# Performance work log

Measured on AMD Instinct MI355X. Metric: run time of the kernel, lower is better.

Reference implementation:

```python
import jax, jax.numpy as jnp
import numpy as np

HIDDEN = 4096
N_HEADS = 32
N_KV_HEADS = 8
HEAD_DIM = HIDDEN // N_HEADS          # 128
GROUP = N_HEADS // N_KV_HEADS         # 4 q-heads per kv-head
Q_SIZE = N_HEADS * HEAD_DIM           # 4096
KV_SIZE = N_KV_HEADS * HEAD_DIM       # 1024
T = 2048


def setup_inputs() -> dict:
    key = jax.random.key(0)
    k1, k2, k3 = jax.random.split(key, 3)
    positions = jnp.arange(T, dtype=jnp.int64) if jax.config.jax_enable_x64 else jnp.arange(T, dtype=jnp.int32)
    hidden_states = jax.random.normal(k1, (T, HIDDEN), dtype=jnp.float32)
    # torch.nn.Linear weights: out = x @ W.T
    w_qkv = jax.random.normal(k2, (Q_SIZE + 2 * KV_SIZE, HIDDEN), dtype=jnp.float32) * 0.02
    w_o = jax.random.normal(k3, (HIDDEN, HIDDEN), dtype=jnp.float32) * 0.02
    return {"positions": positions, "hidden_states": hidden_states, "w_qkv": w_qkv, "w_o": w_o}


def reference(positions, hidden_states, w_qkv, w_o):
    del positions  # rotary is a no-op in the fake module
    t = hidden_states.shape[0]
    scaling = HEAD_DIM ** -0.5

    qkv = hidden_states @ w_qkv.T                              # [T, q+2kv]
    q, k, v = jnp.split(qkv, [Q_SIZE, Q_SIZE + KV_SIZE], axis=-1)
    # GQA mapping: q-head h uses kv-head h // GROUP (contiguous groups)
    q = q.reshape(t, N_KV_HEADS, GROUP, HEAD_DIM)              # [T, Hkv, G, d]
    k = k.reshape(t, N_KV_HEADS, HEAD_DIM)                     # [T, Hkv, d]
    v = v.reshape(t, N_KV_HEADS, HEAD_DIM)

    # Cache starts empty -> token i attends to keys 0..i (causal prefill)
    logits = jnp.einsum('tkgd,skd->kgts', q, k) * scaling      # [Hkv, G, T, T]
    causal = jnp.tril(jnp.ones((t, t), dtype=bool))            # s <= t
    logits = jnp.where(causal, logits, jnp.finfo(logits.dtype).min)
    weights = jax.nn.softmax(logits, axis=-1)
    ctx = jnp.einsum('kgts,skd->tkgd', weights, v)             # [T, Hkv, G, d]
    ctx = ctx.reshape(t, HIDDEN)
    return ctx @ w_o.T
```

## Files before the change

kernel.cpp:

```cpp
#include <hip/hip_runtime.h>

typedef unsigned short u16;
typedef __bf16 bf16x8 __attribute__((ext_vector_type(8)));
typedef float f32x4 __attribute__((ext_vector_type(4)));

__device__ __forceinline__ u16 f2bf(float f) {
  union { float f; unsigned u; } v; v.f = f;
  unsigned r = v.u + 0x7FFFu + ((v.u >> 16) & 1u);
  return (u16)(r >> 16);
}

__device__ __forceinline__ u16 bfc(float f) {
  __bf16 h = (__bf16)f;
  return *(u16*)&h;
}

__device__ __forceinline__ void gload16(const void* g, void* l) {
  __builtin_amdgcn_global_load_lds(
      (const __attribute__((address_space(1))) unsigned int*)g,
      (__attribute__((address_space(3))) unsigned int*)l, 16, 0, 0);
}

__global__ __launch_bounds__(256) void cvt_bf16(const float* __restrict__ in,
                                                u16* __restrict__ out, long n) {
  long i = ((long)blockIdx.x * 256 + threadIdx.x) * 8;
  const long stride = (long)gridDim.x * 2048;
  for (; i < n; i += stride) {
    float4 a = *(const float4*)(in + i);
    float4 b = *(const float4*)(in + i + 4);
    uint4 o;
    o.x = (unsigned)f2bf(a.x) | ((unsigned)f2bf(a.y) << 16);
    o.y = (unsigned)f2bf(a.z) | ((unsigned)f2bf(a.w) << 16);
    o.z = (unsigned)f2bf(b.x) | ((unsigned)f2bf(b.y) << 16);
    o.w = (unsigned)f2bf(b.z) | ((unsigned)f2bf(b.w) << 16);
    *(uint4*)(out + i) = o;
  }
}

__global__ __launch_bounds__(256) void pack_b(const float* __restrict__ w,
                                              u16* __restrict__ out, int kb32) {
  const int tid = threadIdx.x;
  const int unit = blockIdx.x * 4 + (tid >> 6);
  const int ln = tid & 63, lr = ln & 15, lg = ln >> 4;
  const int n16 = unit / kb32, k32 = unit % kb32;
  const float* src = w + (size_t)(n16 * 16 + lr) * (kb32 * 32) + k32 * 32 + lg * 8;
  float4 a = *(const float4*)src;
  float4 b = *(const float4*)(src + 4);
  uint4 o;
  o.x = (unsigned)f2bf(a.x) | ((unsigned)f2bf(a.y) << 16);
  o.y = (unsigned)f2bf(a.z) | ((unsigned)f2bf(a.w) << 16);
  o.z = (unsigned)f2bf(b.x) | ((unsigned)f2bf(b.y) << 16);
  o.w = (unsigned)f2bf(b.z) | ((unsigned)f2bf(b.w) << 16);
  *(uint4*)(out + (size_t)unit * 512 + ln * 8) = o;
}

template <int BN, typename OUT>
__global__ __launch_bounds__(256) void gemmV(const u16* __restrict__ A,
                                             const u16* __restrict__ Bp,
                                             OUT* __restrict__ C,
                                             int M, int N, int K) {
  constexpr int BM = 128;
  constexpr int MREP = 4;
  constexpr int NREP = BN / 32;
  constexpr int AI = 4;
  __shared__ __align__(16) u16 sA[2][BM * 64];

  const int tid = threadIdx.x;
  const int w = tid >> 6, ln = tid & 63;
  const int lr = ln & 15, lg = ln >> 4;
  const int wr = w >> 1, wc = w & 1;

  const int bid = (int)blockIdx.x;
  const int bm = (bid & 15) * BM;
  const int bn = (bid >> 4) * BN;

  const int srow = tid >> 3;
  const int scol = (((tid & 7) * 16) ^ ((srow & 7) << 4)) >> 1;
  const u16* pA = A + (size_t)(bm + srow) * K + scol;

  const int mask = (lr & 7) << 4;
  const int pAr = (wr * 64 + lr) * 128;
  const int kb32 = K >> 5;
  const u16* pB = Bp + ((size_t)((bn >> 4) + wc * NREP)) * kb32 * 512 + ln * 8;

  f32x4 acc[MREP][NREP] = {};
  const int nk = K >> 6;

  auto stageA = [&](int buf, int t) {
    const int k0 = t << 6;
#pragma unroll
    for (int i = 0; i < AI; ++i)
      gload16(pA + (size_t)i * 32 * K + k0, (char*)sA[buf] + i * 4096 + tid * 16);
  };
  auto loadB = [&](bf16x8 (&br)[NREP][2], int t) {
#pragma unroll
    for (int nf = 0; nf < NREP; ++nf)
#pragma unroll
      for (int s = 0; s < 2; ++s)
        br[nf][s] = *(const bf16x8*)(pB + ((size_t)nf * kb32 + 2 * t + s) * 512);
  };

  bf16x8 b[NREP][2];
  stageA(0, 0);
  loadB(b, 0);

#pragma unroll 1
  for (int t = 0; t < nk; ++t) {
    const int buf = t & 1;
    const char* lA = (const char*)sA[buf];
    const bool more = (t + 1 < nk);

    asm volatile("s_waitcnt vmcnt(0)" ::: "memory");
    __builtin_amdgcn_sched_barrier(0);
    __builtin_amdgcn_s_barrier();
    __builtin_amdgcn_sched_barrier(0);
    if (more) stageA(buf ^ 1, t + 1);

    bf16x8 af[MREP][2];
#pragma unroll
    for (int m = 0; m < MREP; ++m)
      af[m][0] = *(const bf16x8*)(lA + pAr + m * 2048 + ((lg * 16) ^ mask));
#pragma unroll
    for (int m = 0; m < MREP; ++m)
      af[m][1] = *(const bf16x8*)(lA + pAr + m * 2048 + ((lg * 16 + 64) ^ mask));

    asm volatile("s_waitcnt lgkmcnt(%0)" :: "n"(MREP) : "memory");
    __builtin_amdgcn_sched_barrier(0);
    __builtin_amdgcn_s_setprio(1);
#pragma unroll
    for (int m = 0; m < MREP; ++m)
#pragma unroll
      for (int nf = 0; nf < NREP; ++nf)
        acc[m][nf] = __builtin_amdgcn_mfma_f32_16x16x32_bf16(
            af[m][0], b[nf][0], acc[m][nf], 0, 0, 0);
    __builtin_amdgcn_s_setprio(0);
    asm volatile("s_waitcnt lgkmcnt(0)" ::: "memory");
    __builtin_amdgcn_sched_barrier(0);
    __builtin_amdgcn_s_setprio(1);
#pragma unroll
    for (int m = 0; m < MREP; ++m)
#pragma unroll
      for (int nf = 0; nf < NREP; ++nf)
        acc[m][nf] = __builtin_amdgcn_mfma_f32_16x16x32_bf16(
            af[m][1], b[nf][1], acc[m][nf], 0, 0, 0);
    __builtin_amdgcn_s_setprio(0);

    if (more) loadB(b, t + 1);
  }

#pragma unroll
  for (int m = 0; m < MREP; ++m)
#pragma unroll
    for (int nf = 0; nf < NREP; ++nf)
#pragma unroll
      for (int r = 0; r < 4; ++r) {
        const int row = bm + wr * 64 + m * 16 + lg * 4 + r;
        const int col = bn + wc * (BN / 2) + nf * 16 + lr;
        const float v = acc[m][nf][r];
        if constexpr (sizeof(OUT) == 2)
          C[(size_t)row * N + col] = (OUT)bfc(v);
        else
          C[(size_t)row * N + col] = v;
      }
}

__global__ __launch_bounds__(256) void vtrans(const u16* __restrict__ qkv,
                                              u16* __restrict__ vT) {
  __shared__ u16 tile[128][65];
  const int hk = blockIdx.y;
  const int tb = blockIdx.x * 64;
  const int tid = threadIdx.x;
#pragma unroll
  for (int p = 0; p < 4; ++p) {
    const int tr = p * 16 + (tid >> 4);
    const int d0 = (tid & 15) * 8;
    const uint4 x = *(const uint4*)(qkv + (size_t)(tb + tr) * 6144 + 5120 + hk * 128 + d0);
    const u16* xv = (const u16*)&x;
#pragma unroll
    for (int j = 0; j < 8; ++j) tile[d0 + j][tr] = xv[j];
  }
  __syncthreads();
#pragma unroll
  for (int p = 0; p < 4; ++p) {
    const int d = p * 32 + (tid >> 3);
    const int t0 = (tid & 7) * 8;
    u16 v[8];
#pragma unroll
    for (int j = 0; j < 8; ++j) v[j] = tile[d][t0 + j];
    uint4 o;
    unsigned* ov = (unsigned*)&o;
#pragma unroll
    for (int j = 0; j < 4; ++j)
      ov[j] = (unsigned)v[2 * j] | ((unsigned)v[2 * j + 1] << 16);
    *(uint4*)(vT + (size_t)hk * 128 * 2048 + (size_t)d * 2048 + tb + t0) = o;
  }
}

__global__ __launch_bounds__(256) void attn(const u16* __restrict__ qkv,
                                            const u16* __restrict__ vT,
                                            u16* __restrict__ ctx) {
  __shared__ __align__(16) u16 sK[2][64 * 128];
  __shared__ __align__(16) u16 sV[2][128 * 64];
  __shared__ __align__(16) u16 sP[4 * 16 * 64];
  const int tid = threadIdx.x, w = tid >> 6, ln = tid & 63;
  const int lr = ln & 15, lg = ln >> 4;
  const int h = blockIdx.y, hk = h >> 2;
  const int pi = blockIdx.x;

  const float Cs = 0.12751737f;
  char* const pw = (char*)sP + w * 2048;

  auto stage = [&](int buf, int kt) {
    const int kvbase = kt * 64;
#pragma unroll
    for (int i = 0; i < 4; ++i) {
      const int off = i * 4096 + tid * 16;
      {
        const int row = off >> 8, cbp = off & 255;
        const int cb = cbp ^ ((row & 7) << 4);
        gload16(qkv + (size_t)(kvbase + row) * 6144 + 4096 + hk * 128 + (cb >> 1),
                (char*)sK + buf * 16384 + off);
      }
      {
        const int row = off >> 7, cbp = off & 127;
        const int cb = cbp ^ ((row & 7) << 4);
        gload16(vT + (size_t)hk * 262144 + (size_t)row * 2048 + kvbase + (cb >> 1),
                (char*)sV + buf * 16384 + off);
      }
    }
  };

#pragma unroll 1
  for (int ph = 0; ph < 2; ++ph) {
    const int qt = ph ? (31 - pi) : pi;
    const int qbase = qt * 64;
    const int nkt = qt + 1;

    bf16x8 qf[4];
    {
      const u16* qrow = qkv + (size_t)(qbase + w * 16 + lr) * 6144 + h * 128 + lg * 8;
#pragma unroll
      for (int kk = 0; kk < 4; ++kk) qf[kk] = *(const bf16x8*)(qrow + kk * 32);
    }

    f32x4 acc_o[8] = {};
    float l_p[4] = {0.f, 0.f, 0.f, 0.f};

    stage(0, 0);

#pragma unroll 1
    for (int kt = 0; kt < nkt; ++kt) {
      const int buf = kt & 1;
      const int kvbase = kt * 64;
      __syncthreads();
      if (kt + 1 < nkt) stage(buf ^ 1, kt + 1);

      char* const kbase = (char*)sK + buf * 16384;
      char* const vbase = (char*)sV + buf * 16384;

      f32x4 sacc[4] = {};
#pragma unroll
      for (int kk = 0; kk < 4; ++kk) {
#pragma unroll
        for (int nf = 0; nf < 4; ++nf) {
          const int row = nf * 16 + lr;
          const int byt = row * 256 + ((kk * 64 + lg * 16) ^ ((row & 7) << 4));
          const bf16x8 kf = *(const bf16x8*)(kbase + byt);
          sacc[nf] = __builtin_amdgcn_mfma_f32_16x16x32_bf16(qf[kk], kf, sacc[nf], 0, 0, 0);
        }
      }

      const bool diag = (kt == qt);
      float p[4][4];
#pragma unroll
      for (int r = 0; r < 4; ++r) {
        const int qrow = qbase + w * 16 + lg * 4 + r;
        float rs = 0.f;
#pragma unroll
        for (int nf = 0; nf < 4; ++nf) {
          const bool masked = diag && (kvbase + nf * 16 + lr > qrow);
          const float e = masked ? 0.f : exp2f(sacc[nf][r] * Cs);
          p[nf][r] = e;
          rs += e;
        }
        l_p[r] += rs;
      }

#pragma unroll
      for (int r = 0; r < 4; ++r) {
        const int row = lg * 4 + r;
#pragma unroll
        for (int nf = 0; nf < 4; ++nf) {
          const int col = nf * 16 + lr;
          const int byt = row * 128 + ((2 * col) ^ ((row & 7) << 4));
          *(u16*)(pw + byt) = bfc(p[nf][r]);
        }
      }

#pragma unroll
      for (int kk2 = 0; kk2 < 2; ++kk2) {
        const int pbyt = lr * 128 + ((kk2 * 64 + lg * 16) ^ ((lr & 7) << 4));
        const bf16x8 pf = *(const bf16x8*)(pw + pbyt);
#pragma unroll
        for (int o = 0; o < 8; ++o) {
          const int vrow = o * 16 + lr;
          const int vbyt = vrow * 128 + ((kk2 * 64 + lg * 16) ^ ((vrow & 7) << 4));
          const bf16x8 vf = *(const bf16x8*)(vbase + vbyt);
          acc_o[o] = __builtin_amdgcn_mfma_f32_16x16x32_bf16(pf, vf, acc_o[o], 0, 0, 0);
        }
      }
    }

#pragma unroll
    for (int r = 0; r < 4; ++r) {
      float l = l_p[r];
      l += __shfl_xor(l, 1);
      l += __shfl_xor(l, 2);
      l += __shfl_xor(l, 4);
      l += __shfl_xor(l, 8);
      const float inv = 1.f / l;
      const int t = qbase + w * 16 + lg * 4 + r;
#pragma unroll
      for (int o = 0; o < 8; ++o)
        ctx[(size_t)t * 4096 + h * 128 + o * 16 + lr] = bfc(acc_o[o][r] * inv);
    }
    __syncthreads();
  }
}

extern "C" void kernel_launch(void* const* d_in, const int* in_sizes, int n_in,
                              void* d_out, int out_size, void* d_ws, size_t ws_size,
                              hipStream_t stream) {
  (void)in_sizes; (void)n_in; (void)out_size; (void)ws_size;
  const float* hidden = (const float*)d_in[1];
  const float* w_qkv = (const float*)d_in[2];
  const float* w_o = (const float*)d_in[3];
  float* out = (float*)d_out;
  char* ws = (char*)d_ws;

  u16* xb    = (u16*)(ws + 0);
  u16* wqkvp = (u16*)(ws + 16777216);
  u16* wop   = (u16*)(ws + 67108864);
  u16* qkvb  = (u16*)(ws + 100663296);
  u16* vTb   = (u16*)(ws + 125829120);
  u16* ctxb  = (u16*)(ws + 130023424);

  cvt_bf16<<<4096, 256, 0, stream>>>(hidden, xb, (long)2048 * 4096);
  pack_b<<<12288, 256, 0, stream>>>(w_qkv, wqkvp, 128);
  pack_b<<<8192, 256, 0, stream>>>(w_o, wop, 128);
  gemmV<192, u16><<<512, 256, 0, stream>>>(xb, wqkvp, qkvb, 2048, 6144, 4096);
  vtrans<<<dim3(32, 8), 256, 0, stream>>>(qkvb, vTb);
  attn<<<dim3(16, 32), 256, 0, stream>>>(qkvb, vTb, ctxb);
  gemmV<128, float><<<512, 256, 0, stream>>>(ctxb, wop, out, 2048, 4096, 4096);
}
```

Measured before the change: 312.3 us.

## Prepack K into MFMA fragment layout and load directly to registers in attention

```diff
diff --git a/kernel.cpp b/kernel.cpp
--- a/kernel.cpp
+++ b/kernel.cpp
@@ -54,6 +54,20 @@
   *(uint4*)(out + (size_t)unit * 512 + ln * 8) = o;
 }
 
+__global__ __launch_bounds__(256) void pack_k(const u16* __restrict__ qkv,
+                                              u16* __restrict__ out) {
+  const int tid = threadIdx.x;
+  const int unit = blockIdx.x * 4 + (tid >> 6);
+  const int ln = tid & 63, lr = ln & 15, lg = ln >> 4;
+  const int hk = unit >> 9;
+  const int t16 = (unit >> 2) & 127;
+  const int d32 = unit & 3;
+  const u16* src = qkv + (size_t)(t16 * 16 + lr) * 6144 + 4096 + hk * 128 +
+                   d32 * 32 + lg * 8;
+  uint4 x = *(const uint4*)src;
+  *(uint4*)(out + (size_t)unit * 512 + ln * 8) = x;
+}
+
 template <int BN, typename OUT>
 __global__ __launch_bounds__(256) void gemmV(const u16* __restrict__ A,
                                              const u16* __restrict__ Bp,
@@ -70,9 +84,9 @@
   const int lr = ln & 15, lg = ln >> 4;
   const int wr = w >> 1, wc = w & 1;
 
-  const int bid = (int)blockIdx.x;
-  const int bm = (bid & 15) * BM;
-  const int bn = (bid >> 4) * BN;
+  const int nN = N / BN;
+  const int bm = ((int)blockIdx.x / nN) * BM;
+  const int bn = ((int)blockIdx.x % nN) * BN;
 
   const int srow = tid >> 3;
   const int scol = (((tid & 7) * 16) ^ ((srow & 7) << 4)) >> 1;
@@ -197,9 +211,9 @@
 }
 
 __global__ __launch_bounds__(256) void attn(const u16* __restrict__ qkv,
+                                            const u16* __restrict__ Kp,
                                             const u16* __restrict__ vT,
                                             u16* __restrict__ ctx) {
-  __shared__ __align__(16) u16 sK[2][64 * 128];
   __shared__ __align__(16) u16 sV[2][128 * 64];
   __shared__ __align__(16) u16 sP[4 * 16 * 64];
   const int tid = threadIdx.x, w = tid >> 6, ln = tid & 63;
@@ -210,23 +224,15 @@
   const float Cs = 0.12751737f;
   char* const pw = (char*)sP + w * 2048;
 
-  auto stage = [&](int buf, int kt) {
+  auto stageV = [&](int buf, int kt) {
     const int kvbase = kt * 64;
 #pragma unroll
     for (int i = 0; i < 4; ++i) {
       const int off = i * 4096 + tid * 16;
-      {
-        const int row = off >> 8, cbp = off & 255;
-        const int cb = cbp ^ ((row & 7) << 4);
-        gload16(qkv + (size_t)(kvbase + row) * 6144 + 4096 + hk * 128 + (cb >> 1),
-                (char*)sK + buf * 16384 + off);
-      }
-      {
-        const int row = off >> 7, cbp = off & 127;
-        const int cb = cbp ^ ((row & 7) << 4);
-        gload16(vT + (size_t)hk * 262144 + (size_t)row * 2048 + kvbase + (cb >> 1),
-                (char*)sV + buf * 16384 + off);
-      }
+      const int row = off >> 7, cbp = off & 127;
+      const int cb = cbp ^ ((row & 7) << 4);
+      gload16(vT + (size_t)hk * 262144 + (size_t)row * 2048 + kvbase + (cb >> 1),
+              (char*)sV + buf * 16384 + off);
     }
   };
 
@@ -246,29 +252,39 @@
     f32x4 acc_o[8] = {};
     float l_p[4] = {0.f, 0.f, 0.f, 0.f};
 
-    stage(0, 0);
+    stageV(0, 0);
 
 #pragma unroll 1
     for (int kt = 0; kt < nkt; ++kt) {
       const int buf = kt & 1;
       const int kvbase = kt * 64;
       __syncthreads();
-      if (kt + 1 < nkt) stage(buf ^ 1, kt + 1);
-
-      char* const kbase = (char*)sK + buf * 16384;
-      char* const vbase = (char*)sV + buf * 16384;
+
+      bf16x8 kf[4][4];
+#pragma unroll
+      for (int nf = 0; nf < 4; ++nf)
+#pragma unroll
+        for (int kk = 0; kk < 4; ++kk)
+          kf[nf][kk] = *(const bf16x8*)(
+              Kp + ((size_t)(hk * 128 + kt * 4 + nf) * 4 + kk) * 512 + ln * 8);
+      const bool more = (kt + 1 < nkt);
+      if (more) {
+        stageV(buf ^ 1, kt + 1);
+        asm volatile("s_waitcnt vmcnt(4)" ::: "memory");
+      } else {
+        asm volatile("s_waitcnt vmcnt(0)" ::: "memory");
+      }
+      __builtin_amdgcn_sched_barrier(0);
 
       f32x4 sacc[4] = {};
-#pragma unroll
-      for (int kk = 0; kk < 4; ++kk) {
-#pragma unroll
-        for (int nf = 0; nf < 4; ++nf) {
-          const int row = nf * 16 + lr;
-          const int byt = row * 256 + ((kk * 64 + lg * 16) ^ ((row & 7) << 4));
-          const bf16x8 kf = *(const bf16x8*)(kbase + byt);
-          sacc[nf] = __builtin_amdgcn_mfma_f32_16x16x32_bf16(qf[kk], kf, sacc[nf], 0, 0, 0);
-        }
-      }
+      __builtin_amdgcn_s_setprio(1);
+#pragma unroll
+      for (int kk = 0; kk < 4; ++kk)
+#pragma unroll
+        for (int nf = 0; nf < 4; ++nf)
+          sacc[nf] = __builtin_amdgcn_mfma_f32_16x16x32_bf16(
+              qf[kk], kf[nf][kk], sacc[nf], 0, 0, 0);
+      __builtin_amdgcn_s_setprio(0);
 
       const bool diag = (kt == qt);
       float p[4][4];
@@ -297,6 +313,7 @@
         }
       }
 
+      char* const vbase = (char*)sV + buf * 16384;
 #pragma unroll
       for (int kk2 = 0; kk2 < 2; ++kk2) {
         const int pbyt = lr * 128 + ((kk2 * 64 + lg * 16) ^ ((lr & 7) << 4));
@@ -344,12 +361,14 @@
   u16* qkvb  = (u16*)(ws + 100663296);
   u16* vTb   = (u16*)(ws + 125829120);
   u16* ctxb  = (u16*)(ws + 130023424);
+  u16* Kp    = wqkvp;
 
   cvt_bf16<<<4096, 256, 0, stream>>>(hidden, xb, (long)2048 * 4096);
   pack_b<<<12288, 256, 0, stream>>>(w_qkv, wqkvp, 128);
   pack_b<<<8192, 256, 0, stream>>>(w_o, wop, 128);
   gemmV<192, u16><<<512, 256, 0, stream>>>(xb, wqkvp, qkvb, 2048, 6144, 4096);
+  pack_k<<<1024, 256, 0, stream>>>(qkvb, Kp);
   vtrans<<<dim3(32, 8), 256, 0, stream>>>(qkvb, vTb);
-  attn<<<dim3(16, 32), 256, 0, stream>>>(qkvb, vTb, ctxb);
+  attn<<<dim3(16, 32), 256, 0, stream>>>(qkvb, Kp, vTb, ctxb);
   gemmV<128, float><<<512, 256, 0, stream>>>(ctxb, wop, out, 2048, 4096, 4096);
 }
```

Result: no change. 316.8 us (+1.4%).

## Double-buffer B fragments in registers and reorder block tile mapping

Applied to the files above, without the earlier changes.

```diff
diff --git a/kernel.cpp b/kernel.cpp
--- a/kernel.cpp
+++ b/kernel.cpp
@@ -70,9 +70,9 @@
   const int lr = ln & 15, lg = ln >> 4;
   const int wr = w >> 1, wc = w & 1;
 
-  const int bid = (int)blockIdx.x;
-  const int bm = (bid & 15) * BM;
-  const int bn = (bid >> 4) * BN;
+  const int nN = N / BN;
+  const int bm = ((int)blockIdx.x / nN) * BM;
+  const int bn = ((int)blockIdx.x % nN) * BN;
 
   const int srow = tid >> 3;
   const int scol = (((tid & 7) * 16) ^ ((srow & 7) << 4)) >> 1;
@@ -99,23 +99,7 @@
       for (int s = 0; s < 2; ++s)
         br[nf][s] = *(const bf16x8*)(pB + ((size_t)nf * kb32 + 2 * t + s) * 512);
   };
-
-  bf16x8 b[NREP][2];
-  stageA(0, 0);
-  loadB(b, 0);
-
-#pragma unroll 1
-  for (int t = 0; t < nk; ++t) {
-    const int buf = t & 1;
-    const char* lA = (const char*)sA[buf];
-    const bool more = (t + 1 < nk);
-
-    asm volatile("s_waitcnt vmcnt(0)" ::: "memory");
-    __builtin_amdgcn_sched_barrier(0);
-    __builtin_amdgcn_s_barrier();
-    __builtin_amdgcn_sched_barrier(0);
-    if (more) stageA(buf ^ 1, t + 1);
-
+  auto compute = [&](const char* lA, bf16x8 (&br)[NREP][2]) {
     bf16x8 af[MREP][2];
 #pragma unroll
     for (int m = 0; m < MREP; ++m)
@@ -123,7 +107,6 @@
 #pragma unroll
     for (int m = 0; m < MREP; ++m)
       af[m][1] = *(const bf16x8*)(lA + pAr + m * 2048 + ((lg * 16 + 64) ^ mask));
-
     asm volatile("s_waitcnt lgkmcnt(%0)" :: "n"(MREP) : "memory");
     __builtin_amdgcn_sched_barrier(0);
     __builtin_amdgcn_s_setprio(1);
@@ -132,7 +115,7 @@
 #pragma unroll
       for (int nf = 0; nf < NREP; ++nf)
         acc[m][nf] = __builtin_amdgcn_mfma_f32_16x16x32_bf16(
-            af[m][0], b[nf][0], acc[m][nf], 0, 0, 0);
+            af[m][0], br[nf][0], acc[m][nf], 0, 0, 0);
     __builtin_amdgcn_s_setprio(0);
     asm volatile("s_waitcnt lgkmcnt(0)" ::: "memory");
     __builtin_amdgcn_sched_barrier(0);
@@ -142,10 +125,32 @@
 #pragma unroll
       for (int nf = 0; nf < NREP; ++nf)
         acc[m][nf] = __builtin_amdgcn_mfma_f32_16x16x32_bf16(
-            af[m][1], b[nf][1], acc[m][nf], 0, 0, 0);
+            af[m][1], br[nf][1], acc[m][nf], 0, 0, 0);
     __builtin_amdgcn_s_setprio(0);
-
-    if (more) loadB(b, t + 1);
+  };
+
+  bf16x8 bE[NREP][2], bO[NREP][2];
+  stageA(0, 0);
+  loadB(bE, 0);
+
+#pragma unroll 1
+  for (int t = 0; t < nk; t += 2) {
+    asm volatile("s_waitcnt vmcnt(0)" ::: "memory");
+    __builtin_amdgcn_sched_barrier(0);
+    __builtin_amdgcn_s_barrier();
+    __builtin_amdgcn_sched_barrier(0);
+    const bool m1 = (t + 1 < nk);
+    if (m1) { stageA(1, t + 1); loadB(bO, t + 1); }
+    compute((const char*)sA[0], bE);
+
+    if (!m1) break;
+    asm volatile("s_waitcnt vmcnt(0)" ::: "memory");
+    __builtin_amdgcn_sched_barrier(0);
+    __builtin_amdgcn_s_barrier();
+    __builtin_amdgcn_sched_barrier(0);
+    const bool m2 = (t + 2 < nk);
+    if (m2) { stageA(0, t + 2); loadB(bE, t + 2); }
+    compute((const char*)sA[1], bO);
   }
 
 #pragma unroll
```

New measurement: 399.5 us. +27.9%, slower.
